# Kernel tuning notes

Hardware: AMD Instinct MI355X
Metric: run time of the kernel (lower is better)

Reference implementation:

```python
import jax, jax.numpy as jnp
import numpy as np

HEADS = 8

def setup_inputs() -> dict:
    key = jax.random.key(0)
    ks = jax.random.split(key, 4)
    b, n, d = 4, 4097, 128  # n = 64*64 + 1 (CLS + spatial)
    x = jax.random.normal(ks[0], (b, n, d), dtype=jnp.float32)
    W_qkv = jax.random.normal(ks[1], (d, 3 * d), dtype=jnp.float32) * (d ** -0.5)
    b_qkv = jnp.zeros((3 * d,), dtype=jnp.float32)
    W_out = jax.random.normal(ks[2], (d, d), dtype=jnp.float32) * (d ** -0.5)
    b_out = jnp.zeros((d,), dtype=jnp.float32)
    return {"x": x, "W_qkv": W_qkv, "b_qkv": b_qkv, "W_out": W_out, "b_out": b_out}

def reference(x, W_qkv, b_qkv, W_out, b_out):
    b, n, d = x.shape
    h = HEADS
    dh = d // h
    scale = d ** -0.5  # note: module scales by dim**-0.5, not head_dim**-0.5
    qkv = x @ W_qkv + b_qkv                      # [b, n, 3d]
    q, k, v = jnp.split(qkv, 3, axis=-1)
    def to_heads(t):
        return t.reshape(b, n, h, dh).transpose(0, 2, 1, 3)  # [b, h, n, dh]
    q, k, v = to_heads(q), to_heads(k), to_heads(v)
    dots = jnp.einsum('bhid,bhjd->bhij', q, k) * scale       # [b, h, n, n]
    attn = jax.nn.softmax(dots, axis=-1)
    out = jnp.einsum('bhij,bhjd->bhid', attn, v)             # [b, h, n, dh]
    out = out.transpose(0, 2, 1, 3).reshape(b, n, d)
    return out @ W_out + b_out
```

## Files before the change

kernel.cpp:

```cpp
#include <hip/hip_runtime.h>
#include <hip/hip_bf16.h>
#include <stdint.h>


#define BB 4
#define NN 4097
#define NNP 4112
#define DD 128
#define HH 8
#define DH 16
#define BH (BB*HH)
#define ROWS (BB*NN)
#define MT  1025
#define NSP 4

typedef _Float16 h4 __attribute__((ext_vector_type(4)));
typedef _Float16 h8 __attribute__((ext_vector_type(8)));
typedef __fp16   fp16v2 __attribute__((ext_vector_type(2)));
typedef float    f4 __attribute__((ext_vector_type(4)));

#define QSCALE (0.08838834764831845f * 1.4426950408889634f)

#if __has_builtin(__builtin_amdgcn_exp2f)
#define EXP2F(x) __builtin_amdgcn_exp2f(x)
#else
#define EXP2F(x) exp2f(x)
#endif

union H4u { h4 v; fp16v2 p[2]; };
union H8u { h8 v; fp16v2 p[4]; };

static __device__ __forceinline__ H4u pack4u(float a, float b, float c, float d) {
    H4u u;
#if __has_builtin(__builtin_amdgcn_cvt_pkrtz)
    u.p[0] = __builtin_amdgcn_cvt_pkrtz(a, b);
    u.p[1] = __builtin_amdgcn_cvt_pkrtz(c, d);
#else
    u.v[0] = (_Float16)a; u.v[1] = (_Float16)b; u.v[2] = (_Float16)c; u.v[3] = (_Float16)d;
#endif
    return u;
}

static __device__ __forceinline__ h8 pack8u(const float4& t0, const float4& t1) {
    H8u u;
#if __has_builtin(__builtin_amdgcn_cvt_pkrtz)
    u.p[0] = __builtin_amdgcn_cvt_pkrtz(t0.x, t0.y);
    u.p[1] = __builtin_amdgcn_cvt_pkrtz(t0.z, t0.w);
    u.p[2] = __builtin_amdgcn_cvt_pkrtz(t1.x, t1.y);
    u.p[3] = __builtin_amdgcn_cvt_pkrtz(t1.z, t1.w);
#else
    u.v[0]=(_Float16)t0.x; u.v[1]=(_Float16)t0.y; u.v[2]=(_Float16)t0.z; u.v[3]=(_Float16)t0.w;
    u.v[4]=(_Float16)t1.x; u.v[5]=(_Float16)t1.y; u.v[6]=(_Float16)t1.z; u.v[7]=(_Float16)t1.w;
#endif
    return u.v;
}

__global__ __launch_bounds__(256) void prep(
    const float* __restrict__ Wqkv,
    const float* __restrict__ Wout,
    _Float16* __restrict__ WqkvT,
    _Float16* __restrict__ WoutT)
{
    const int id = blockIdx.x*256 + threadIdx.x;
    if (id < 384*128) {
        const int n = id >> 7, k = id & 127;
        const float s = (n < 128) ? QSCALE : 1.0f;
        WqkvT[id] = (_Float16)(Wqkv[k*384 + n] * s);
    } else if (id < 384*128 + 128*128) {
        const int e = id - 384*128;
        const int n = e >> 7, k = e & 127;
        WoutT[e] = (_Float16)(Wout[k*128 + n]);
    }
}

__global__ __launch_bounds__(256) void qkv_mfma(
    const float* __restrict__ x,
    const _Float16* __restrict__ WqkvT,
    const float* __restrict__ bqkv,
    _Float16* __restrict__ Qh,
    _Float16* __restrict__ Kh,
    _Float16* __restrict__ Vt)
{
    __shared__ _Float16 tile[16][264];
    const int wid  = blockIdx.x;
    const int wave = threadIdx.x >> 6;
    const int lane = threadIdx.x & 63;
    const int quad = lane >> 4, l16 = lane & 15;

    const int rowlo = wid*16;
    const int blo   = rowlo / NN;
    const bool vfast = (rowlo + 15 < ROWS) && (rowlo + 15 - blo*NN < NN);
    const int nrow0 = rowlo - blo*NN;

    const int arow = rowlo + l16;
    const int arc  = (arow < ROWS) ? arow : (ROWS - 1);
    const float* xr = x + (size_t)arc*DD;
    h8 af[4];
    #pragma unroll
    for (int kk = 0; kk < 4; ++kk) {
        const float4 t0 = *(const float4*)(xr + kk*32 + quad*8);
        const float4 t1 = *(const float4*)(xr + kk*32 + quad*8 + 4);
        af[kk] = pack8u(t0, t1);
    }

    const int nt0 = wave*6;

    for (int nt = nt0; nt < nt0 + 6; nt += 2) {
        const float b0 = bqkv[nt*16 + l16]      * ((nt   < 8) ? QSCALE : 1.0f);
        const float b1 = bqkv[nt*16 + 16 + l16] * ((nt+1 < 8) ? QSCALE : 1.0f);
        f4 a0 = {b0,b0,b0,b0}, a1 = {b1,b1,b1,b1};
        #pragma unroll
        for (int kk = 0; kk < 4; ++kk) {
            const h8 bf0 = *(const h8*)(WqkvT + (size_t)(nt*16      + l16)*DD + kk*32 + quad*8);
            const h8 bf1 = *(const h8*)(WqkvT + (size_t)(nt*16 + 16 + l16)*DD + kk*32 + quad*8);
            a0 = __builtin_amdgcn_mfma_f32_16x16x32_f16(af[kk], bf0, a0, 0, 0, 0);
            a1 = __builtin_amdgcn_mfma_f32_16x16x32_f16(af[kk], bf1, a1, 0, 0, 0);
        }
        #pragma unroll
        for (int u = 0; u < 2; ++u) {
            const int ntc = nt + u;
            const f4 av = u ? a1 : a0;
            if (ntc < 16) {
                #pragma unroll
                for (int r = 0; r < 4; ++r)
                    tile[quad*4 + r][ntc*16 + l16] = (_Float16)av[r];
            } else {
                const int head = ntc & 7;
                if (vfast) {
                    h4 pk;
                    pk[0] = (_Float16)av[0]; pk[1] = (_Float16)av[1];
                    pk[2] = (_Float16)av[2]; pk[3] = (_Float16)av[3];
                    *(h4*)(Vt + ((size_t)(blo*HH + head)*DH + l16)*NNP + nrow0 + quad*4) = pk;
                } else {
                    #pragma unroll
                    for (int r = 0; r < 4; ++r) {
                        const int row = rowlo + quad*4 + r;
                        if (row < ROWS) {
                            const int bidx = row / NN;
                            const int nrow = row - bidx*NN;
                            Vt[((size_t)(bidx*HH + head)*DH + l16)*NNP + nrow] = (_Float16)av[r];
                        }
                    }
                }
            }
        }
    }
    __syncthreads();

    {
        const int u   = threadIdx.x;
        const int ntc = u >> 4, lt = u & 15;
        const int row = rowlo + lt;
        if (row < ROWS) {
            _Float16* base = (ntc < 8) ? Qh : Kh;
            const int head = ntc & 7;
            const int bidx = row / NN;
            const int nrow = row - bidx*NN;
            _Float16* dst = base + ((size_t)(bidx*HH + head)*NNP + nrow)*DH;
            *(h8*)dst       = *(const h8*)&tile[lt][ntc*16];
            *(h8*)(dst + 8) = *(const h8*)&tile[lt][ntc*16 + 8];
        }
    }
}

__global__ __launch_bounds__(256, 8) void attn_mfma(
    const _Float16* __restrict__ Qh,
    const _Float16* __restrict__ Kh,
    const _Float16* __restrict__ Vt,
    _Float16* __restrict__ PACC,
    float* __restrict__ PL)
{
    const int qt   = blockIdx.x;
    const int bh   = blockIdx.y;
    const int sp   = blockIdx.z;
    const int tid  = threadIdx.x;
    const int wave = tid >> 6;
    const int lane = tid & 63;
    const int quad = lane >> 4;
    const int l16  = lane & 15;
    const int bidx = bh >> 3, head = bh & 7;

    const int qbase = qt*256 + wave*64;

    const _Float16* Qb = Qh + (size_t)bh*NNP*DH;
    h4 qf[4];
    #pragma unroll
    for (int g = 0; g < 4; ++g) {
        const int qr = qbase + g*16 + l16;
        const int qc = (qr < NN) ? qr : (NN-1);
        qf[g] = *(const h4*)(Qb + (size_t)qc*DH + quad*4);
    }

    f4 acc[4] = {{0,0,0,0},{0,0,0,0},{0,0,0,0},{0,0,0,0}};
    float ls[4] = {0.f,0.f,0.f,0.f};

    const int t0 = sp*64;
    const int t1 = t0 + 64;

    const _Float16* kp = Kh + ((size_t)bh*NNP + (size_t)t0*16 + l16)*DH + quad*4;
    const _Float16* vp = Vt + ((size_t)bh*DH + l16)*NNP + t0*16 + quad*4;

    h4 ak = *(const h4*)kp;
    h4 av = *(const h4*)vp;
    const f4 zero = {0.f,0.f,0.f,0.f};
#if __has_builtin(__builtin_amdgcn_fdot2)
    const fp16v2 one2 = {(__fp16)1.0f, (__fp16)1.0f};
#endif

    for (int tt = t0; tt < t1; ++tt) {
        kp += 16*DH; vp += 16;
        const h4 nak = *(const h4*)kp;
        const h4 nav = *(const h4*)vp;
        #pragma unroll
        for (int g = 0; g < 4; ++g) {
            f4 d = __builtin_amdgcn_mfma_f32_16x16x16f16(ak, qf[g], zero, 0, 0, 0);
            const float p0 = EXP2F(d[0]), p1 = EXP2F(d[1]), p2 = EXP2F(d[2]), p3 = EXP2F(d[3]);
            const H4u pb = pack4u(p0, p1, p2, p3);
#if __has_builtin(__builtin_amdgcn_fdot2)
            ls[g] = __builtin_amdgcn_fdot2(pb.p[0], one2,
                     __builtin_amdgcn_fdot2(pb.p[1], one2, ls[g], false), false);
#else
            ls[g] += (p0 + p1) + (p2 + p3);
#endif
            acc[g] = __builtin_amdgcn_mfma_f32_16x16x16f16(av, pb.v, acc[g], 0, 0, 0);
        }
        ak = nak; av = nav;
    }

    if (sp == 3) {
        #pragma unroll
        for (int g = 0; g < 4; ++g) {
            f4 d = __builtin_amdgcn_mfma_f32_16x16x16f16(ak, qf[g], zero, 0, 0, 0);
            const float p0 = (quad == 0) ? EXP2F(d[0]) : 0.f;
            ls[g] += p0;
            const H4u pb = pack4u(p0, 0.f, 0.f, 0.f);
            acc[g] = __builtin_amdgcn_mfma_f32_16x16x16f16(av, pb.v, acc[g], 0, 0, 0);
        }
    }

    const size_t rb = (size_t)sp*ROWS + (size_t)bidx*NN;
    #pragma unroll
    for (int g = 0; g < 4; ++g) {
        float l = ls[g];
        l += __shfl_xor(l, 16);
        l += __shfl_xor(l, 32);
        const int qr = qbase + g*16 + l16;
        if (qr < NN) {
            const float inv = 1.0f / l;
            const H4u st = pack4u(acc[g][0]*inv, acc[g][1]*inv, acc[g][2]*inv, acc[g][3]*inv);
            *(h4*)(PACC + (rb + qr)*DD + head*DH + quad*4) = st.v;
            if (quad == 0) PL[(rb + qr)*HH + head] = l;
        }
    }
}

__global__ __launch_bounds__(256) void out_mfma(
    const _Float16* __restrict__ PACC,
    const float* __restrict__ PL,
    const _Float16* __restrict__ WoutT,
    const float* __restrict__ bout,
    float* __restrict__ out)
{
    __shared__ _Float16 afl[16][136];
    const int wid  = blockIdx.x;
    const int tid  = threadIdx.x;
    const int wave = tid >> 6;
    const int lane = tid & 63;
    const int quad = lane >> 4, l16 = lane & 15;
    const int nt   = wave*2;

    h8 wf[2][4];
    #pragma unroll
    for (int u = 0; u < 2; ++u)
        #pragma unroll
        for (int kk = 0; kk < 4; ++kk)
            wf[u][kk] = *(const h8*)(WoutT + (size_t)((nt+u)*16 + l16)*DD + kk*32 + quad*8);
    const float b0 = bout[nt*16 + l16];
    const float b1 = bout[nt*16 + 16 + l16];

    {
        const int t   = tid >> 4;
        const int seg = tid & 15;
        const int head = seg >> 1;
        const int arow = wid*16 + t;
        const int arc  = (arow < ROWS) ? arow : (ROWS - 1);
        float l[NSP], lsum = 0.f;
        #pragma unroll
        for (int sp = 0; sp < NSP; ++sp) {
            l[sp] = PL[((size_t)sp*ROWS + arc)*HH + head];
            lsum += l[sp];
        }
        const float inv = 1.0f / lsum;
        float m[8] = {0,0,0,0,0,0,0,0};
        #pragma unroll
        for (int sp = 0; sp < NSP; ++sp) {
            const float s = l[sp]*inv;
            const h8 p = *(const h8*)(PACC + ((size_t)sp*ROWS + arc)*DD + seg*8);
            #pragma unroll
            for (int j = 0; j < 8; ++j) m[j] += s*(float)p[j];
        }
        H8u u;
#if __has_builtin(__builtin_amdgcn_cvt_pkrtz)
        u.p[0] = __builtin_amdgcn_cvt_pkrtz(m[0], m[1]);
        u.p[1] = __builtin_amdgcn_cvt_pkrtz(m[2], m[3]);
        u.p[2] = __builtin_amdgcn_cvt_pkrtz(m[4], m[5]);
        u.p[3] = __builtin_amdgcn_cvt_pkrtz(m[6], m[7]);
#else
        #pragma unroll
        for (int j = 0; j < 8; ++j) u.v[j] = (_Float16)m[j];
#endif
        *(h8*)&afl[t][seg*8] = u.v;
    }
    __syncthreads();

    h8 af[4];
    #pragma unroll
    for (int kk = 0; kk < 4; ++kk)
        af[kk] = *(const h8*)&afl[l16][kk*32 + quad*8];

    f4 a0 = {b0,b0,b0,b0}, a1 = {b1,b1,b1,b1};
    #pragma unroll
    for (int kk = 0; kk < 4; ++kk) {
        a0 = __builtin_amdgcn_mfma_f32_16x16x32_f16(af[kk], wf[0][kk], a0, 0, 0, 0);
        a1 = __builtin_amdgcn_mfma_f32_16x16x32_f16(af[kk], wf[1][kk], a1, 0, 0, 0);
    }
    const int r0 = wid*16 + quad*4;
    #pragma unroll
    for (int r = 0; r < 4; ++r) {
        const int row = r0 + r;
        if (row < ROWS) {
            out[(size_t)row*DD + nt*16      + l16] = a0[r];
            out[(size_t)row*DD + nt*16 + 16 + l16] = a1[r];
        }
    }
}

extern "C" void kernel_launch(void* const* d_in, const int* in_sizes, int n_in,
                              void* d_out, int out_size, void* d_ws, size_t ws_size,
                              hipStream_t stream) {
    const float* x    = (const float*)d_in[0];
    const float* Wqkv = (const float*)d_in[1];
    const float* bqkv = (const float*)d_in[2];
    const float* Wout = (const float*)d_in[3];
    const float* bout = (const float*)d_in[4];
    for (int i = 0; i < n_in; ++i) {
        switch (in_sizes[i]) {
            case 2097664: x    = (const float*)d_in[i]; break;
            case 49152:   Wqkv = (const float*)d_in[i]; break;
            case 384:     bqkv = (const float*)d_in[i]; break;
            case 16384:   Wout = (const float*)d_in[i]; break;
            case 128:     bout = (const float*)d_in[i]; break;
            default: break;
        }
    }
    float* out = (float*)d_out;

    const size_t perh = (size_t)BH * NNP * DH;
    _Float16* Qh   = (_Float16*)d_ws;
    _Float16* Kh   = Qh + perh;
    _Float16* Vt   = Kh + perh;
    _Float16* PACC = Vt + perh;
    float*    PL    = (float*)(PACC + (size_t)NSP*ROWS*DD);
    _Float16* WqkvT = (_Float16*)(PL + (size_t)NSP*ROWS*HH);
    _Float16* WoutT = WqkvT + 384*128;

    const int prep_total = 384*128 + 128*128;

    hipLaunchKernelGGL(prep, dim3((prep_total + 255)/256), dim3(256), 0, stream,
                       Wqkv, Wout, WqkvT, WoutT);
    hipLaunchKernelGGL(qkv_mfma, dim3(MT), dim3(256), 0, stream,
                       x, WqkvT, bqkv, Qh, Kh, Vt);
    hipLaunchKernelGGL(attn_mfma, dim3(17, BH, NSP), dim3(256), 0, stream,
                       Qh, Kh, Vt, PACC, PL);
    hipLaunchKernelGGL(out_mfma, dim3(MT), dim3(256), 0, stream,
                       PACC, PL, WoutT, bout, out);
}
```

Baseline: 176.2 us.

## Split KV range across waves within block and reduce partials in shared memory

The attention kernel now assigns each block 64 query rows, and its four waves each process a quarter of the keys. Partial accumulators and row sums are combined through shared memory before a single normalized fp16 output is written. This removes the global split-K partial buffers and the combine step in the output projection, which now reads the attention result directly from global memory. The cost is shared-memory traffic, a block barrier, and more blocks that each reload Q.

Result: slower. 194.0 us (+10.1%).

```diff
diff --git a/kernel.cpp b/kernel.cpp
--- a/kernel.cpp
+++ b/kernel.cpp
@@ -12,7 +12,6 @@
 #define BH (BB*HH)
 #define ROWS (BB*NN)
 #define MT  1025
-#define NSP 4
 
 typedef _Float16 h4 __attribute__((ext_vector_type(4)));
 typedef _Float16 h8 __attribute__((ext_vector_type(8)));
@@ -167,12 +166,12 @@
     const _Float16* __restrict__ Qh,
     const _Float16* __restrict__ Kh,
     const _Float16* __restrict__ Vt,
-    _Float16* __restrict__ PACC,
-    float* __restrict__ PL)
+    _Float16* __restrict__ PACC)
 {
-    const int qt   = blockIdx.x;
+    __shared__ float accs[4][4][16][17];
+    __shared__ float lsl[4][4][17];
+    const int qblk = blockIdx.x;
     const int bh   = blockIdx.y;
-    const int sp   = blockIdx.z;
     const int tid  = threadIdx.x;
     const int wave = tid >> 6;
     const int lane = tid & 63;
@@ -180,7 +179,7 @@
     const int l16  = lane & 15;
     const int bidx = bh >> 3, head = bh & 7;
 
-    const int qbase = qt*256 + wave*64;
+    const int qbase = qblk*64;
 
     const _Float16* Qb = Qh + (size_t)bh*NNP*DH;
     h4 qf[4];
@@ -194,7 +193,7 @@
     f4 acc[4] = {{0,0,0,0},{0,0,0,0},{0,0,0,0},{0,0,0,0}};
     float ls[4] = {0.f,0.f,0.f,0.f};
 
-    const int t0 = sp*64;
+    const int t0 = wave*64;
     const int t1 = t0 + 64;
 
     const _Float16* kp = Kh + ((size_t)bh*NNP + (size_t)t0*16 + l16)*DH + quad*4;
@@ -227,7 +226,7 @@
         ak = nak; av = nav;
     }
 
-    if (sp == 3) {
+    if (wave == 3) {
         #pragma unroll
         for (int g = 0; g < 4; ++g) {
             f4 d = __builtin_amdgcn_mfma_f32_16x16x16f16(ak, qf[g], zero, 0, 0, 0);
@@ -238,34 +237,47 @@
         }
     }
 
-    const size_t rb = (size_t)sp*ROWS + (size_t)bidx*NN;
     #pragma unroll
     for (int g = 0; g < 4; ++g) {
         float l = ls[g];
         l += __shfl_xor(l, 16);
         l += __shfl_xor(l, 32);
+        if (quad == 0) lsl[wave][g][l16] = l;
+        #pragma unroll
+        for (int r = 0; r < 4; ++r)
+            accs[wave][g][quad*4 + r][l16] = acc[g][r];
+    }
+    __syncthreads();
+
+    {
+        const int g = wave;
         const int qr = qbase + g*16 + l16;
         if (qr < NN) {
-            const float inv = 1.0f / l;
-            const H4u st = pack4u(acc[g][0]*inv, acc[g][1]*inv, acc[g][2]*inv, acc[g][3]*inv);
-            *(h4*)(PACC + (rb + qr)*DD + head*DH + quad*4) = st.v;
-            if (quad == 0) PL[(rb + qr)*HH + head] = l;
+            float o[4] = {0.f,0.f,0.f,0.f};
+            float lt = 0.f;
+            #pragma unroll
+            for (int w = 0; w < 4; ++w) {
+                lt += lsl[w][g][l16];
+                #pragma unroll
+                for (int r = 0; r < 4; ++r)
+                    o[r] += accs[w][g][quad*4 + r][l16];
+            }
+            const float inv = 1.0f / lt;
+            const H4u st = pack4u(o[0]*inv, o[1]*inv, o[2]*inv, o[3]*inv);
+            *(h4*)(PACC + ((size_t)bidx*NN + qr)*DD + head*DH + quad*4) = st.v;
         }
     }
 }
 
 __global__ __launch_bounds__(256) void out_mfma(
     const _Float16* __restrict__ PACC,
-    const float* __restrict__ PL,
     const _Float16* __restrict__ WoutT,
     const float* __restrict__ bout,
     float* __restrict__ out)
 {
-    __shared__ _Float16 afl[16][136];
     const int wid  = blockIdx.x;
-    const int tid  = threadIdx.x;
-    const int wave = tid >> 6;
-    const int lane = tid & 63;
+    const int wave = threadIdx.x >> 6;
+    const int lane = threadIdx.x & 63;
     const int quad = lane >> 4, l16 = lane & 15;
     const int nt   = wave*2;
 
@@ -278,45 +290,12 @@
     const float b0 = bout[nt*16 + l16];
     const float b1 = bout[nt*16 + 16 + l16];
 
-    {
-        const int t   = tid >> 4;
-        const int seg = tid & 15;
-        const int head = seg >> 1;
-        const int arow = wid*16 + t;
-        const int arc  = (arow < ROWS) ? arow : (ROWS - 1);
-        float l[NSP], lsum = 0.f;
-        #pragma unroll
-        for (int sp = 0; sp < NSP; ++sp) {
-            l[sp] = PL[((size_t)sp*ROWS + arc)*HH + head];
-            lsum += l[sp];
-        }
-        const float inv = 1.0f / lsum;
-        float m[8] = {0,0,0,0,0,0,0,0};
-        #pragma unroll
-        for (int sp = 0; sp < NSP; ++sp) {
-            const float s = l[sp]*inv;
-            const h8 p = *(const h8*)(PACC + ((size_t)sp*ROWS + arc)*DD + seg*8);
-            #pragma unroll
-            for (int j = 0; j < 8; ++j) m[j] += s*(float)p[j];
-        }
-        H8u u;
-#if __has_builtin(__builtin_amdgcn_cvt_pkrtz)
-        u.p[0] = __builtin_amdgcn_cvt_pkrtz(m[0], m[1]);
-        u.p[1] = __builtin_amdgcn_cvt_pkrtz(m[2], m[3]);
-        u.p[2] = __builtin_amdgcn_cvt_pkrtz(m[4], m[5]);
-        u.p[3] = __builtin_amdgcn_cvt_pkrtz(m[6], m[7]);
-#else
-        #pragma unroll
-        for (int j = 0; j < 8; ++j) u.v[j] = (_Float16)m[j];
-#endif
-        *(h8*)&afl[t][seg*8] = u.v;
-    }
-    __syncthreads();
-
+    const int arow = wid*16 + l16;
+    const int arc  = (arow < ROWS) ? arow : (ROWS - 1);
     h8 af[4];
     #pragma unroll
     for (int kk = 0; kk < 4; ++kk)
-        af[kk] = *(const h8*)&afl[l16][kk*32 + quad*8];
+        af[kk] = *(const h8*)(PACC + (size_t)arc*DD + kk*32 + quad*8);
 
     f4 a0 = {b0,b0,b0,b0}, a1 = {b1,b1,b1,b1};
     #pragma unroll
@@ -360,8 +339,7 @@
     _Float16* Kh   = Qh + perh;
     _Float16* Vt   = Kh + perh;
     _Float16* PACC = Vt + perh;
-    float*    PL    = (float*)(PACC + (size_t)NSP*ROWS*DD);
-    _Float16* WqkvT = (_Float16*)(PL + (size_t)NSP*ROWS*HH);
+    _Float16* WqkvT = PACC + (size_t)ROWS*DD;
     _Float16* WoutT = WqkvT + 384*128;
 
     const int prep_total = 384*128 + 128*128;
@@ -370,8 +348,8 @@
                        Wqkv, Wout, WqkvT, WoutT);
     hipLaunchKernelGGL(qkv_mfma, dim3(MT), dim3(256), 0, stream,
                        x, WqkvT, bqkv, Qh, Kh, Vt);
-    hipLaunchKernelGGL(attn_mfma, dim3(17, BH, NSP), dim3(256), 0, stream,
-                       Qh, Kh, Vt, PACC, PL);
+    hipLaunchKernelGGL(attn_mfma, dim3(65, BH), dim3(256), 0, stream,
+                       Qh, Kh, Vt, PACC);
     hipLaunchKernelGGL(out_mfma, dim3(MT), dim3(256), 0, stream,
-                       PACC, PL, WoutT, bout, out);
-}
+                       PACC, WoutT, bout, out);
+}
```
